# Kernel tuning notes

Measured on AMD Instinct MI355X. Metric: run time of the kernel, lower is better.

The kernel has to match this reference:

```python
import jax, jax.numpy as jnp
import numpy as np

N = 500_000      # num nodes
E = 8_000_000    # num edges (before self-loops)
F_IN, H, C = 16, 8, 2


def setup_inputs() -> dict:
    key = jax.random.key(0)
    k = jax.random.split(key, 6)
    x = jax.random.normal(k[0], (N, F_IN), dtype=jnp.float32)
    edge_index = jax.random.randint(k[1], (2, E), 0, N, dtype=jnp.int32)
    # Glorot-style init like PyG GCNConv
    W1 = jax.random.normal(k[2], (F_IN, H), dtype=jnp.float32) * (1.0 / np.sqrt(F_IN))
    b1 = jnp.zeros((H,), dtype=jnp.float32)
    W2 = jax.random.normal(k[3], (H, C), dtype=jnp.float32) * (1.0 / np.sqrt(H))
    b2 = jnp.zeros((C,), dtype=jnp.float32)
    return {"x": x, "W1": W1, "b1": b1, "W2": W2, "b2": b2, "edge_index": edge_index}


def reference(x, W1, b1, W2, b2, edge_index):
    # GCNConv: out = D^{-1/2} (A + I) D^{-1/2} X W + b   (PyG semantics)
    row, col = edge_index[0], edge_index[1]           # messages flow row -> col
    loop = jnp.arange(N, dtype=row.dtype)
    row = jnp.concatenate([row, loop])                # add self-loops
    col = jnp.concatenate([col, loop])
    deg = jax.ops.segment_sum(jnp.ones_like(col, dtype=x.dtype), col, num_segments=N)
    dinv = jnp.where(deg > 0, jax.lax.rsqrt(deg), jnp.zeros_like(deg))
    norm = dinv[row] * dinv[col]                      # [E+N]

    def propagate(h):  # h: [N, d] -> normalized scatter-add aggregation
        msg = h[row] * norm[:, None]                  # gather + scale, [E+N, d]
        return jax.ops.segment_sum(msg, col, num_segments=N)

    h = jax.nn.relu(propagate(x @ W1) + b1)           # [N, 8]
    out = propagate(h @ W2) + b2                      # [N, 2]
    return jax.nn.log_softmax(out, axis=1)
```

## Files before the change

### kernel.cpp

```cpp
#include <hip/hip_runtime.h>

#define TPB 256
#define NBLK_EDGE 1024
#define CHUNKE 8192
#define BIN_SHIFT 9
#define BIN_SIZE 512
#define MAXK 1024
#define ROW_BITS 19
#define ROW_MASK ((1u << ROW_BITS) - 1)
#define Q_SHIFT 17
#define NKEY 2048
#define CAP 12288

typedef _Float16 half8  __attribute__((ext_vector_type(8)));
typedef _Float16 half2v __attribute__((ext_vector_type(2)));

__global__ void k_hist(const int* __restrict__ col, int E, int chunk, int K,
                       int* __restrict__ cntB, int* __restrict__ cntT) {
    __shared__ int lh[MAXK];
    int blk = blockIdx.x;
    for (int k = threadIdx.x; k < MAXK; k += blockDim.x) lh[k] = 0;
    __syncthreads();
    int s = blk * chunk, e_ = min(s + chunk, E);
    for (int e = s + threadIdx.x; e < e_; e += blockDim.x)
        atomicAdd(&lh[col[e] >> BIN_SHIFT], 1);
    __syncthreads();
    for (int k = threadIdx.x; k < MAXK; k += blockDim.x) {
        int v = lh[k];
        cntB[(size_t)blk * MAXK + k] = v;
        cntT[(size_t)k * NBLK_EDGE + blk] = v;
    }
}

__global__ void k_colscan(int* __restrict__ cntT, int* __restrict__ ghist) {
    __shared__ int part[256];
    int b = blockIdx.x, tid = threadIdx.x;
    size_t base = (size_t)b * NBLK_EDGE;
    int t4 = tid * 4;
    int c0 = cntT[base + t4], c1 = cntT[base + t4 + 1],
        c2 = cntT[base + t4 + 2], c3 = cntT[base + t4 + 3];
    int sum = c0 + c1 + c2 + c3;
    part[tid] = sum;
    __syncthreads();
    for (int off = 1; off < 256; off <<= 1) {
        int v = (tid >= off) ? part[tid - off] : 0;
        __syncthreads();
        part[tid] += v;
        __syncthreads();
    }
    int excl = part[tid] - sum;
    cntT[base + t4]     = excl;
    cntT[base + t4 + 1] = excl + c0;
    cntT[base + t4 + 2] = excl + c0 + c1;
    cntT[base + t4 + 3] = excl + c0 + c1 + c2;
    if (tid == 255) ghist[b] = part[255];
}

__global__ void k_scan(const int* __restrict__ ghist, int K, int* __restrict__ binBase,
                       int* __restrict__ scratchCur) {
    __shared__ int tmp[MAXK];
    int tid = threadIdx.x;
    if (tid == 0) *scratchCur = 0;
    int val = (tid < K) ? ghist[tid] : 0;
    tmp[tid] = val;
    __syncthreads();
    for (int off = 1; off < MAXK; off <<= 1) {
        int v = (tid >= off) ? tmp[tid - off] : 0;
        __syncthreads();
        tmp[tid] += v;
        __syncthreads();
    }
    int incl = tmp[tid];
    if (tid < K) binBase[tid] = incl - val;
    if (tid == K - 1) binBase[K] = incl;
}

__global__ void __launch_bounds__(1024) k_reorder(
        const int* __restrict__ row, const int* __restrict__ col,
        int E, int chunk, int K,
        const int* __restrict__ binBase, const int* __restrict__ cntB,
        const int* __restrict__ cntT, unsigned* __restrict__ packed) {
    __shared__ unsigned sorted[CHUNKE];
    __shared__ unsigned short sbin[CHUNKE];
    __shared__ int lcur[MAXK], lbase[MAXK], gbase[MAXK];
    __shared__ int part[1024];
    int blk = blockIdx.x, tid = threadIdx.x;
    int s = blk * chunk, e_ = min(s + chunk, E), len = e_ - s;
    size_t bb = (size_t)blk * MAXK;
    int c0 = cntB[bb + tid];
    part[tid] = c0;
    __syncthreads();
    for (int off = 1; off < 1024; off <<= 1) {
        int v = (tid >= off) ? part[tid - off] : 0;
        __syncthreads();
        part[tid] += v;
        __syncthreads();
    }
    int excl = part[tid] - c0;
    lbase[tid] = excl;
    lcur[tid] = excl;
    gbase[tid] = binBase[tid] + cntT[(size_t)tid * NBLK_EDGE + blk];
    __syncthreads();
    for (int i = tid; i < len; i += blockDim.x) {
        int cc = col[s + i];
        int b = cc >> BIN_SHIFT;
        int slot = atomicAdd(&lcur[b], 1);
        sorted[slot] = ((unsigned)(cc & (BIN_SIZE - 1)) << ROW_BITS) | (unsigned)row[s + i];
        sbin[slot] = (unsigned short)b;
    }
    __syncthreads();
    for (int i = tid; i < len; i += blockDim.x) {
        int b = sbin[i];
        packed[gbase[b] + (i - lbase[b])] = sorted[i];
    }
}

__global__ void __launch_bounds__(1024) k_binsort_deg(
        unsigned* __restrict__ packed, const int* __restrict__ binBase,
        unsigned* __restrict__ scratch, int* __restrict__ scratchCur,
        const float* __restrict__ x, const float* __restrict__ W1,
        float* __restrict__ dinv, half8* __restrict__ g0,
        int* __restrict__ keyptr, int N, int E, int K) {
    __shared__ unsigned buf2[CAP];
    __shared__ int cnt[NKEY], cur[NKEY];
    __shared__ int part[1024];
    __shared__ int sbShared;
    int tid = threadIdx.x;
    int bin = blockIdx.x;
    int s = binBase[bin], t = binBase[bin + 1];
    int len = t - s;
    bool fast = (len <= CAP);
    cnt[tid] = 0;
    cnt[tid + 1024] = 0;
    if (!fast && tid == 0) sbShared = atomicAdd(scratchCur, len);
    __syncthreads();
    for (int i = tid; i < len; i += blockDim.x) {
        unsigned v = packed[s + i];
        int k = (int)((v >> ROW_BITS) << 2) | (int)((v & ROW_MASK) >> Q_SHIFT);
        atomicAdd(&cnt[k], 1);
    }
    __syncthreads();
    int t2 = tid * 2;
    int c0 = cnt[t2], c1 = cnt[t2 + 1];
    int sum = c0 + c1;
    part[tid] = sum;
    __syncthreads();
    for (int off = 1; off < 1024; off <<= 1) {
        int v = (tid >= off) ? part[tid - off] : 0;
        __syncthreads();
        part[tid] += v;
        __syncthreads();
    }
    int excl = part[tid] - sum;
    cur[t2] = excl;
    cur[t2 + 1] = excl + c0;
    int base = bin << BIN_SHIFT;
    if (base + (t2 >> 2) < N) keyptr[((size_t)bin << 11) + t2] = s + excl;
    if (base + ((t2 + 1) >> 2) < N) keyptr[((size_t)bin << 11) + t2 + 1] = s + excl + c0;
    float di = 0.0f;
    int node = base + tid;
    if (tid < BIN_SIZE && node < N) {
        int deg = cnt[4 * tid] + cnt[4 * tid + 1] + cnt[4 * tid + 2] + cnt[4 * tid + 3];
        di = rsqrtf((float)(deg + 1));
        dinv[node] = di;
    }
    if (bin == K - 1 && tid == 0) keyptr[(size_t)4 * N] = E;
    __syncthreads();
    if (fast) {
        for (int i = tid; i < len; i += blockDim.x) {
            unsigned v = packed[s + i];
            int k = (int)((v >> ROW_BITS) << 2) | (int)((v & ROW_MASK) >> Q_SHIFT);
            int slot = atomicAdd(&cur[k], 1);
            buf2[slot] = v;
        }
        __syncthreads();
        for (int i = tid; i < len; i += blockDim.x) packed[s + i] = buf2[i];
    } else {
        unsigned* stg = scratch + sbShared;
        for (int i = tid; i < len; i += blockDim.x) stg[i] = packed[s + i];
        __threadfence();
        __syncthreads();
        for (int i = tid; i < len; i += blockDim.x) {
            unsigned v = stg[i];
            int k = (int)((v >> ROW_BITS) << 2) | (int)((v & ROW_MASK) >> Q_SHIFT);
            int slot = atomicAdd(&cur[k], 1);
            packed[s + slot] = v;
        }
    }
    if (tid < BIN_SIZE && node < N) {
        const float4* xv = (const float4*)(x + (size_t)node * 16);
        float h[8];
#pragma unroll
        for (int j = 0; j < 8; ++j) h[j] = 0.0f;
#pragma unroll
        for (int kk = 0; kk < 4; ++kk) {
            float4 a = xv[kk];
            int kb = kk * 4;
#pragma unroll
            for (int j = 0; j < 8; ++j)
                h[j] += a.x * W1[kb * 8 + j] + a.y * W1[(kb + 1) * 8 + j]
                      + a.z * W1[(kb + 2) * 8 + j] + a.w * W1[(kb + 3) * 8 + j];
        }
        half8 g;
#pragma unroll
        for (int j = 0; j < 8; ++j) g[j] = (_Float16)(di * h[j]);
        g0[node] = g;
    }
}

__global__ void k_gather1_phase(const unsigned* __restrict__ packed,
                                const int* __restrict__ keyptr,
                                const half8* __restrict__ g0,
                                const float* __restrict__ dinv_arr,
                                const float* __restrict__ b1,
                                const float* __restrict__ W2,
                                float* __restrict__ accA,
                                half2v* __restrict__ g1, int N, int q) {
    int i = blockIdx.x * blockDim.x + threadIdx.x;
    if (i >= N) return;
    int s = keyptr[4 * i + q], t = keyptr[4 * i + q + 1];
    float acc[8];
    if (q == 0) {
#pragma unroll
        for (int j = 0; j < 8; ++j) acc[j] = 0.0f;
    } else {
        const float4* av = (const float4*)(accA + (size_t)i * 8);
        float4 lo = av[0], hi = av[1];
        acc[0] = lo.x; acc[1] = lo.y; acc[2] = lo.z; acc[3] = lo.w;
        acc[4] = hi.x; acc[5] = hi.y; acc[6] = hi.z; acc[7] = hi.w;
    }
    int e = s;
    for (; e + 4 <= t; e += 4) {
        unsigned p0 = packed[e], p1 = packed[e + 1], p2 = packed[e + 2], p3 = packed[e + 3];
        half8 v0 = g0[p0 & ROW_MASK];
        half8 v1 = g0[p1 & ROW_MASK];
        half8 v2 = g0[p2 & ROW_MASK];
        half8 v3 = g0[p3 & ROW_MASK];
#pragma unroll
        for (int j = 0; j < 8; ++j)
            acc[j] += (float)v0[j] + (float)v1[j] + (float)v2[j] + (float)v3[j];
    }
    for (; e < t; ++e) {
        half8 v = g0[packed[e] & ROW_MASK];
#pragma unroll
        for (int j = 0; j < 8; ++j) acc[j] += (float)v[j];
    }
    if (q < 3) {
        float4* av = (float4*)(accA + (size_t)i * 8);
        av[0] = make_float4(acc[0], acc[1], acc[2], acc[3]);
        av[1] = make_float4(acc[4], acc[5], acc[6], acc[7]);
    } else {
        half8 self = g0[i];
        float di = dinv_arr[i];
        float o0 = 0.0f, o1 = 0.0f;
#pragma unroll
        for (int j = 0; j < 8; ++j) {
            float hj = fmaxf(di * (acc[j] + (float)self[j]) + b1[j], 0.0f);
            o0 += hj * W2[j * 2 + 0];
            o1 += hj * W2[j * 2 + 1];
        }
        half2v g;
        g.x = (_Float16)(di * o0);
        g.y = (_Float16)(di * o1);
        g1[i] = g;
    }
}

__global__ void k_gather2_final(const unsigned* __restrict__ packed,
                                const int* __restrict__ keyptr,
                                const half2v* __restrict__ g1,
                                const float* __restrict__ dinv_arr,
                                const float* __restrict__ b2,
                                float* __restrict__ out, int N) {
    int i = blockIdx.x * blockDim.x + threadIdx.x;
    if (i >= N) return;
    int s = keyptr[4 * i], t = keyptr[4 * i + 4];
    half2v sg = g1[i];
    float a0 = (float)sg.x, a1 = (float)sg.y;
    int e = s;
    for (; e + 4 <= t; e += 4) {
        unsigned p0 = packed[e], p1 = packed[e + 1], p2 = packed[e + 2], p3 = packed[e + 3];
        half2v v0 = g1[p0 & ROW_MASK];
        half2v v1 = g1[p1 & ROW_MASK];
        half2v v2 = g1[p2 & ROW_MASK];
        half2v v3 = g1[p3 & ROW_MASK];
        a0 += (float)v0.x + (float)v1.x + (float)v2.x + (float)v3.x;
        a1 += (float)v0.y + (float)v1.y + (float)v2.y + (float)v3.y;
    }
    for (; e < t; ++e) {
        half2v v = g1[packed[e] & ROW_MASK];
        a0 += (float)v.x;
        a1 += (float)v.y;
    }
    float di = dinv_arr[i];
    float o0 = di * a0 + b2[0];
    float o1 = di * a1 + b2[1];
    float m = fmaxf(o0, o1);
    float lse = m + logf(expf(o0 - m) + expf(o1 - m));
    ((float2*)out)[i] = make_float2(o0 - lse, o1 - lse);
}

extern "C" void kernel_launch(void* const* d_in, const int* in_sizes, int n_in,
                              void* d_out, int out_size, void* d_ws, size_t ws_size,
                              hipStream_t stream) {
    const float* x  = (const float*)d_in[0];
    const float* W1 = (const float*)d_in[1];
    const float* b1 = (const float*)d_in[2];
    const float* W2 = (const float*)d_in[3];
    const float* b2 = (const float*)d_in[4];
    const int*   ei = (const int*)d_in[5];

    const int N = in_sizes[0] / 16;
    const int E = in_sizes[5] / 2;
    const int* row = ei;
    const int* col = ei + E;
    const int K = (N + BIN_SIZE - 1) >> BIN_SHIFT;

    float* ws   = (float*)d_ws;
    float* dinv = ws;
    half8* g0   = (half8*)(ws + (size_t)N);
    half2v* g1  = (half2v*)(ws + (size_t)5 * N);
    float* accA = ws + (size_t)6 * N;
    int* keyptr = (int*)(ws + (size_t)14 * N);
    int*   meta = (int*)(ws + (size_t)18 * N + 8);
    int* ghist      = meta;
    int* binBase    = meta + MAXK;
    int* scratchCur = meta + 2 * MAXK + 16;
    unsigned* packed = (unsigned*)(meta + 3 * MAXK);
    int* cntB = (int*)(packed + E);
    int* cntT = cntB + (size_t)MAXK * NBLK_EDGE;

    float* out = (float*)d_out;

    const int gN = (N + TPB - 1) / TPB;
    const int chunk = (E + NBLK_EDGE - 1) / NBLK_EDGE;

    k_hist       <<<NBLK_EDGE, TPB, 0, stream>>>(col, E, chunk, K, cntB, cntT);
    k_colscan    <<<K, 256, 0, stream>>>(cntT, ghist);
    k_scan       <<<1, MAXK, 0, stream>>>(ghist, K, binBase, scratchCur);
    k_reorder    <<<NBLK_EDGE, 1024, 0, stream>>>(row, col, E, chunk, K,
                                                  binBase, cntB, cntT, packed);
    k_binsort_deg<<<K, 1024, 0, stream>>>(packed, binBase, (unsigned*)accA, scratchCur,
                                          x, W1, dinv, g0, keyptr, N, E, K);
    for (int q = 0; q < 4; ++q)
        k_gather1_phase<<<gN, TPB, 0, stream>>>(packed, keyptr, g0, dinv, b1, W2,
                                                accA, g1, N, q);
    k_gather2_final<<<gN, TPB, 0, stream>>>(packed, keyptr, g1, dinv, b2, out, N);
}
```

Measured before the change: 371.9 us.

## Fuse gather phases into one cooperative kernel and use wave-shuffle block scans

Replaces the four per-quarter gather launches and the final gather with one cooperative kernel. It keeps accumulators in registers across grid.sync barriers, recomputes dinv from keyptr, and runs the second propagation plus log_softmax in the same kernel. This removes the accA global read/write round trips and several launches. The Hillis-Steele shared-memory scans become wave-shuffle scans, and the edge-chunk block count is halved with bigger chunks and 1024-thread histogram blocks. The cost is grid-wide barriers, and the kernel relies on every block being co-resident; if occupancy is too low it falls back to the old path.

Result: faster. 356.7 us (-4.1%).

```diff
diff --git a/kernel.cpp b/kernel.cpp
--- a/kernel.cpp
+++ b/kernel.cpp
@@ -1,8 +1,11 @@
 #include <hip/hip_runtime.h>
+#include <hip/hip_cooperative_groups.h>
+
+namespace cg = cooperative_groups;
 
 #define TPB 256
-#define NBLK_EDGE 1024
-#define CHUNKE 8192
+#define NBLK_EDGE 512
+#define CHUNKE 16384
 #define BIN_SHIFT 9
 #define BIN_SIZE 512
 #define MAXK 1024
@@ -15,6 +18,33 @@
 typedef _Float16 half8  __attribute__((ext_vector_type(8)));
 typedef _Float16 half2v __attribute__((ext_vector_type(2)));
 
+__device__ __forceinline__ int wave_scan_incl(int v, int lane) {
+#pragma unroll
+    for (int d = 1; d < 64; d <<= 1) {
+        int u = __shfl_up(v, d, 64);
+        if (lane >= d) v += u;
+    }
+    return v;
+}
+
+__device__ __forceinline__ int block_excl_scan_1024(int v, int tid, int* wsum) {
+    int lane = tid & 63, wv = tid >> 6;
+    int incl = wave_scan_incl(v, lane);
+    if (lane == 63) wsum[wv] = incl;
+    __syncthreads();
+    if (tid < 16) {
+        int w = wsum[tid];
+#pragma unroll
+        for (int d = 1; d < 16; d <<= 1) {
+            int u = __shfl_up(w, d, 16);
+            if (tid >= d) w += u;
+        }
+        wsum[tid] = w;
+    }
+    __syncthreads();
+    return incl - v + (wv ? wsum[wv - 1] : 0);
+}
+
 __global__ void k_hist(const int* __restrict__ col, int E, int chunk, int K,
                        int* __restrict__ cntB, int* __restrict__ cntT) {
     __shared__ int lh[MAXK];
@@ -36,10 +66,9 @@
     __shared__ int part[256];
     int b = blockIdx.x, tid = threadIdx.x;
     size_t base = (size_t)b * NBLK_EDGE;
-    int t4 = tid * 4;
-    int c0 = cntT[base + t4], c1 = cntT[base + t4 + 1],
-        c2 = cntT[base + t4 + 2], c3 = cntT[base + t4 + 3];
-    int sum = c0 + c1 + c2 + c3;
+    int t2 = tid * 2;
+    int c0 = cntT[base + t2], c1 = cntT[base + t2 + 1];
+    int sum = c0 + c1;
     part[tid] = sum;
     __syncthreads();
     for (int off = 1; off < 256; off <<= 1) {
@@ -49,30 +78,20 @@
         __syncthreads();
     }
     int excl = part[tid] - sum;
-    cntT[base + t4]     = excl;
-    cntT[base + t4 + 1] = excl + c0;
-    cntT[base + t4 + 2] = excl + c0 + c1;
-    cntT[base + t4 + 3] = excl + c0 + c1 + c2;
+    cntT[base + t2]     = excl;
+    cntT[base + t2 + 1] = excl + c0;
     if (tid == 255) ghist[b] = part[255];
 }
 
 __global__ void k_scan(const int* __restrict__ ghist, int K, int* __restrict__ binBase,
                        int* __restrict__ scratchCur) {
-    __shared__ int tmp[MAXK];
+    __shared__ int wsum[16];
     int tid = threadIdx.x;
     if (tid == 0) *scratchCur = 0;
     int val = (tid < K) ? ghist[tid] : 0;
-    tmp[tid] = val;
-    __syncthreads();
-    for (int off = 1; off < MAXK; off <<= 1) {
-        int v = (tid >= off) ? tmp[tid - off] : 0;
-        __syncthreads();
-        tmp[tid] += v;
-        __syncthreads();
-    }
-    int incl = tmp[tid];
-    if (tid < K) binBase[tid] = incl - val;
-    if (tid == K - 1) binBase[K] = incl;
+    int excl = block_excl_scan_1024(val, tid, wsum);
+    if (tid < K) binBase[tid] = excl;
+    if (tid == K - 1) binBase[K] = excl + val;
 }
 
 __global__ void __launch_bounds__(1024) k_reorder(
@@ -83,20 +102,12 @@
     __shared__ unsigned sorted[CHUNKE];
     __shared__ unsigned short sbin[CHUNKE];
     __shared__ int lcur[MAXK], lbase[MAXK], gbase[MAXK];
-    __shared__ int part[1024];
+    __shared__ int wsum[16];
     int blk = blockIdx.x, tid = threadIdx.x;
     int s = blk * chunk, e_ = min(s + chunk, E), len = e_ - s;
     size_t bb = (size_t)blk * MAXK;
     int c0 = cntB[bb + tid];
-    part[tid] = c0;
-    __syncthreads();
-    for (int off = 1; off < 1024; off <<= 1) {
-        int v = (tid >= off) ? part[tid - off] : 0;
-        __syncthreads();
-        part[tid] += v;
-        __syncthreads();
-    }
-    int excl = part[tid] - c0;
+    int excl = block_excl_scan_1024(c0, tid, wsum);
     lbase[tid] = excl;
     lcur[tid] = excl;
     gbase[tid] = binBase[tid] + cntT[(size_t)tid * NBLK_EDGE + blk];
@@ -123,7 +134,7 @@
         int* __restrict__ keyptr, int N, int E, int K) {
     __shared__ unsigned buf2[CAP];
     __shared__ int cnt[NKEY], cur[NKEY];
-    __shared__ int part[1024];
+    __shared__ int wsum[16];
     __shared__ int sbShared;
     int tid = threadIdx.x;
     int bin = blockIdx.x;
@@ -143,15 +154,7 @@
     int t2 = tid * 2;
     int c0 = cnt[t2], c1 = cnt[t2 + 1];
     int sum = c0 + c1;
-    part[tid] = sum;
-    __syncthreads();
-    for (int off = 1; off < 1024; off <<= 1) {
-        int v = (tid >= off) ? part[tid - off] : 0;
-        __syncthreads();
-        part[tid] += v;
-        __syncthreads();
-    }
-    int excl = part[tid] - sum;
+    int excl = block_excl_scan_1024(sum, tid, wsum);
     cur[t2] = excl;
     cur[t2 + 1] = excl + c0;
     int base = bin << BIN_SHIFT;
@@ -205,6 +208,95 @@
 #pragma unroll
         for (int j = 0; j < 8; ++j) g[j] = (_Float16)(di * h[j]);
         g0[node] = g;
+    }
+}
+
+__device__ __forceinline__ void gather_g0_range(const unsigned* __restrict__ packed,
+                                                const half8* __restrict__ g0,
+                                                int e, int t, float* acc) {
+    for (; e + 4 <= t; e += 4) {
+        unsigned p0 = packed[e], p1 = packed[e + 1], p2 = packed[e + 2], p3 = packed[e + 3];
+        half8 v0 = g0[p0 & ROW_MASK];
+        half8 v1 = g0[p1 & ROW_MASK];
+        half8 v2 = g0[p2 & ROW_MASK];
+        half8 v3 = g0[p3 & ROW_MASK];
+#pragma unroll
+        for (int j = 0; j < 8; ++j)
+            acc[j] += (float)v0[j] + (float)v1[j] + (float)v2[j] + (float)v3[j];
+    }
+    for (; e < t; ++e) {
+        half8 v = g0[packed[e] & ROW_MASK];
+#pragma unroll
+        for (int j = 0; j < 8; ++j) acc[j] += (float)v[j];
+    }
+}
+
+__global__ void __launch_bounds__(TPB, 8) k_gather_fused(
+        const unsigned* __restrict__ packed, const int* __restrict__ keyptr,
+        const half8* __restrict__ g0, const float* __restrict__ b1,
+        const float* __restrict__ W2, const float* __restrict__ b2,
+        half2v* __restrict__ g1, float* __restrict__ out, int N) {
+    cg::grid_group grid = cg::this_grid();
+    int i = blockIdx.x * blockDim.x + threadIdx.x;
+    bool act = (i < N);
+    int kp0 = 0, kp1 = 0, kp2 = 0, kp3 = 0, kp4 = 0;
+    float acc[8];
+#pragma unroll
+    for (int j = 0; j < 8; ++j) acc[j] = 0.0f;
+    if (act) {
+        int4 k4 = ((const int4*)keyptr)[i];
+        kp0 = k4.x; kp1 = k4.y; kp2 = k4.z; kp3 = k4.w;
+        kp4 = keyptr[4 * i + 4];
+    }
+    if (act) gather_g0_range(packed, g0, kp0, kp1, acc);
+    grid.sync();
+    if (act) gather_g0_range(packed, g0, kp1, kp2, acc);
+    grid.sync();
+    if (act) gather_g0_range(packed, g0, kp2, kp3, acc);
+    grid.sync();
+    if (act) gather_g0_range(packed, g0, kp3, kp4, acc);
+    float di = 0.0f, s0 = 0.0f, s1 = 0.0f;
+    if (act) {
+        half8 self = g0[i];
+        di = rsqrtf((float)(kp4 - kp0 + 1));
+        float o0 = 0.0f, o1 = 0.0f;
+#pragma unroll
+        for (int j = 0; j < 8; ++j) {
+            float hj = fmaxf(di * (acc[j] + (float)self[j]) + b1[j], 0.0f);
+            o0 += hj * W2[j * 2 + 0];
+            o1 += hj * W2[j * 2 + 1];
+        }
+        s0 = di * o0;
+        s1 = di * o1;
+        half2v g;
+        g.x = (_Float16)s0;
+        g.y = (_Float16)s1;
+        g1[i] = g;
+    }
+    __threadfence();
+    grid.sync();
+    if (act) {
+        float a0 = s0, a1 = s1;
+        int e = kp0, t = kp4;
+        for (; e + 4 <= t; e += 4) {
+            unsigned p0 = packed[e], p1 = packed[e + 1], p2 = packed[e + 2], p3 = packed[e + 3];
+            half2v v0 = g1[p0 & ROW_MASK];
+            half2v v1 = g1[p1 & ROW_MASK];
+            half2v v2 = g1[p2 & ROW_MASK];
+            half2v v3 = g1[p3 & ROW_MASK];
+            a0 += (float)v0.x + (float)v1.x + (float)v2.x + (float)v3.x;
+            a1 += (float)v0.y + (float)v1.y + (float)v2.y + (float)v3.y;
+        }
+        for (; e < t; ++e) {
+            half2v v = g1[packed[e] & ROW_MASK];
+            a0 += (float)v.x;
+            a1 += (float)v.y;
+        }
+        float o0 = di * a0 + b2[0];
+        float o1 = di * a1 + b2[1];
+        float m = fmaxf(o0, o1);
+        float lse = m + logf(expf(o0 - m) + expf(o1 - m));
+        ((float2*)out)[i] = make_float2(o0 - lse, o1 - lse);
     }
 }
 
@@ -229,22 +321,7 @@
         acc[0] = lo.x; acc[1] = lo.y; acc[2] = lo.z; acc[3] = lo.w;
         acc[4] = hi.x; acc[5] = hi.y; acc[6] = hi.z; acc[7] = hi.w;
     }
-    int e = s;
-    for (; e + 4 <= t; e += 4) {
-        unsigned p0 = packed[e], p1 = packed[e + 1], p2 = packed[e + 2], p3 = packed[e + 3];
-        half8 v0 = g0[p0 & ROW_MASK];
-        half8 v1 = g0[p1 & ROW_MASK];
-        half8 v2 = g0[p2 & ROW_MASK];
-        half8 v3 = g0[p3 & ROW_MASK];
-#pragma unroll
-        for (int j = 0; j < 8; ++j)
-            acc[j] += (float)v0[j] + (float)v1[j] + (float)v2[j] + (float)v3[j];
-    }
-    for (; e < t; ++e) {
-        half8 v = g0[packed[e] & ROW_MASK];
-#pragma unroll
-        for (int j = 0; j < 8; ++j) acc[j] += (float)v[j];
-    }
+    gather_g0_range(packed, g0, s, t, acc);
     if (q < 3) {
         float4* av = (float4*)(accA + (size_t)i * 8);
         av[0] = make_float4(acc[0], acc[1], acc[2], acc[3]);
@@ -335,15 +412,34 @@
     const int gN = (N + TPB - 1) / TPB;
     const int chunk = (E + NBLK_EDGE - 1) / NBLK_EDGE;
 
-    k_hist       <<<NBLK_EDGE, TPB, 0, stream>>>(col, E, chunk, K, cntB, cntT);
+    static int coop_capacity = -1;
+    if (coop_capacity < 0) {
+        int nb = 0;
+        if (hipOccupancyMaxActiveBlocksPerMultiprocessor(&nb, k_gather_fused, TPB, 0)
+            != hipSuccess) nb = 0;
+        hipDeviceProp_t prop;
+        int ncu = 0;
+        if (hipGetDeviceProperties(&prop, 0) == hipSuccess) ncu = prop.multiProcessorCount;
+        coop_capacity = nb * ncu;
+    }
+
+    k_hist       <<<NBLK_EDGE, 1024, 0, stream>>>(col, E, chunk, K, cntB, cntT);
     k_colscan    <<<K, 256, 0, stream>>>(cntT, ghist);
     k_scan       <<<1, MAXK, 0, stream>>>(ghist, K, binBase, scratchCur);
     k_reorder    <<<NBLK_EDGE, 1024, 0, stream>>>(row, col, E, chunk, K,
                                                   binBase, cntB, cntT, packed);
     k_binsort_deg<<<K, 1024, 0, stream>>>(packed, binBase, (unsigned*)accA, scratchCur,
                                           x, W1, dinv, g0, keyptr, N, E, K);
-    for (int q = 0; q < 4; ++q)
-        k_gather1_phase<<<gN, TPB, 0, stream>>>(packed, keyptr, g0, dinv, b1, W2,
-                                                accA, g1, N, q);
-    k_gather2_final<<<gN, TPB, 0, stream>>>(packed, keyptr, g1, dinv, b2, out, N);
-}
+    if (coop_capacity >= gN) {
+        int nN = N;
+        void* cargs[] = {(void*)&packed, (void*)&keyptr, (void*)&g0, (void*)&b1,
+                         (void*)&W2, (void*)&b2, (void*)&g1, (void*)&out, (void*)&nN};
+        hipLaunchCooperativeKernel(k_gather_fused, dim3(gN), dim3(TPB),
+                                   cargs, 0, stream);
+    } else {
+        for (int q = 0; q < 4; ++q)
+            k_gather1_phase<<<gN, TPB, 0, stream>>>(packed, keyptr, g0, dinv, b1, W2,
+                                                    accA, g1, N, q);
+        k_gather2_final<<<gN, TPB, 0, stream>>>(packed, keyptr, g1, dinv, b2, out, N);
+    }
+}
```

## Replace per-node CSR sort with per-bin shared-memory atomic aggregation

Applied to the files above, without the earlier changes.

Drops the second-level within-bin sort and the keyptr CSR. Edges are now only coarsely binned by destination into 1024-node bins, and each bin's block accumulates messages with LDS float atomics for both propagation layers. This removes the binsort pass, the four phased gather launches and the accA round trips. It also swaps the shared-memory Hillis-Steele scans for wave-shuffle scans and retunes chunk and bin sizes. In exchange there are many more LDS atomics (8 per edge in layer 1), and the float summation order is no longer deterministic.

Result: slower. 613.1 us (+64.8%).

```diff
diff --git a/kernel.cpp b/kernel.cpp
--- a/kernel.cpp
+++ b/kernel.cpp
@@ -1,22 +1,46 @@
 #include <hip/hip_runtime.h>
 
-#define TPB 256
-#define NBLK_EDGE 1024
-#define CHUNKE 8192
-#define BIN_SHIFT 9
-#define BIN_SIZE 512
+#define NBLK_EDGE 768
+#define CHUNKE 10432
+#define BIN_SHIFT 10
+#define BIN_SIZE 1024
 #define MAXK 1024
 #define ROW_BITS 19
 #define ROW_MASK ((1u << ROW_BITS) - 1)
-#define Q_SHIFT 17
-#define NKEY 2048
-#define CAP 12288
 
 typedef _Float16 half8  __attribute__((ext_vector_type(8)));
 typedef _Float16 half2v __attribute__((ext_vector_type(2)));
 
-__global__ void k_hist(const int* __restrict__ col, int E, int chunk, int K,
-                       int* __restrict__ cntB, int* __restrict__ cntT) {
+__device__ __forceinline__ int wave_scan_incl(int v, int lane) {
+#pragma unroll
+    for (int d = 1; d < 64; d <<= 1) {
+        int u = __shfl_up(v, d, 64);
+        if (lane >= d) v += u;
+    }
+    return v;
+}
+
+__device__ __forceinline__ int block_excl_scan_1024(int v, int tid, int* wsum) {
+    int lane = tid & 63, wv = tid >> 6;
+    int incl = wave_scan_incl(v, lane);
+    if (lane == 63) wsum[wv] = incl;
+    __syncthreads();
+    if (tid < 16) {
+        int w = wsum[tid];
+#pragma unroll
+        for (int d = 1; d < 16; d <<= 1) {
+            int u = __shfl_up(w, d, 16);
+            if (tid >= d) w += u;
+        }
+        wsum[tid] = w;
+    }
+    __syncthreads();
+    return incl - v + (wv ? wsum[wv - 1] : 0);
+}
+
+__global__ void __launch_bounds__(1024) k_hist(
+        const int* __restrict__ col, int E, int chunk, int K,
+        int* __restrict__ cntB, int* __restrict__ cntT) {
     __shared__ int lh[MAXK];
     int blk = blockIdx.x;
     for (int k = threadIdx.x; k < MAXK; k += blockDim.x) lh[k] = 0;
@@ -36,10 +60,9 @@
     __shared__ int part[256];
     int b = blockIdx.x, tid = threadIdx.x;
     size_t base = (size_t)b * NBLK_EDGE;
-    int t4 = tid * 4;
-    int c0 = cntT[base + t4], c1 = cntT[base + t4 + 1],
-        c2 = cntT[base + t4 + 2], c3 = cntT[base + t4 + 3];
-    int sum = c0 + c1 + c2 + c3;
+    int t3 = tid * 3;
+    int c0 = cntT[base + t3], c1 = cntT[base + t3 + 1], c2 = cntT[base + t3 + 2];
+    int sum = c0 + c1 + c2;
     part[tid] = sum;
     __syncthreads();
     for (int off = 1; off < 256; off <<= 1) {
@@ -49,30 +72,19 @@
         __syncthreads();
     }
     int excl = part[tid] - sum;
-    cntT[base + t4]     = excl;
-    cntT[base + t4 + 1] = excl + c0;
-    cntT[base + t4 + 2] = excl + c0 + c1;
-    cntT[base + t4 + 3] = excl + c0 + c1 + c2;
+    cntT[base + t3]     = excl;
+    cntT[base + t3 + 1] = excl + c0;
+    cntT[base + t3 + 2] = excl + c0 + c1;
     if (tid == 255) ghist[b] = part[255];
 }
 
-__global__ void k_scan(const int* __restrict__ ghist, int K, int* __restrict__ binBase,
-                       int* __restrict__ scratchCur) {
-    __shared__ int tmp[MAXK];
+__global__ void k_scan(const int* __restrict__ ghist, int K, int* __restrict__ binBase) {
+    __shared__ int wsum[16];
     int tid = threadIdx.x;
-    if (tid == 0) *scratchCur = 0;
     int val = (tid < K) ? ghist[tid] : 0;
-    tmp[tid] = val;
-    __syncthreads();
-    for (int off = 1; off < MAXK; off <<= 1) {
-        int v = (tid >= off) ? tmp[tid - off] : 0;
-        __syncthreads();
-        tmp[tid] += v;
-        __syncthreads();
-    }
-    int incl = tmp[tid];
-    if (tid < K) binBase[tid] = incl - val;
-    if (tid == K - 1) binBase[K] = incl;
+    int excl = block_excl_scan_1024(val, tid, wsum);
+    if (tid < K) binBase[tid] = excl;
+    if (tid == K - 1) binBase[K] = excl + val;
 }
 
 __global__ void __launch_bounds__(1024) k_reorder(
@@ -83,20 +95,12 @@
     __shared__ unsigned sorted[CHUNKE];
     __shared__ unsigned short sbin[CHUNKE];
     __shared__ int lcur[MAXK], lbase[MAXK], gbase[MAXK];
-    __shared__ int part[1024];
+    __shared__ int wsum[16];
     int blk = blockIdx.x, tid = threadIdx.x;
     int s = blk * chunk, e_ = min(s + chunk, E), len = e_ - s;
     size_t bb = (size_t)blk * MAXK;
     int c0 = cntB[bb + tid];
-    part[tid] = c0;
-    __syncthreads();
-    for (int off = 1; off < 1024; off <<= 1) {
-        int v = (tid >= off) ? part[tid - off] : 0;
-        __syncthreads();
-        part[tid] += v;
-        __syncthreads();
-    }
-    int excl = part[tid] - c0;
+    int excl = block_excl_scan_1024(c0, tid, wsum);
     lbase[tid] = excl;
     lcur[tid] = excl;
     gbase[tid] = binBase[tid] + cntT[(size_t)tid * NBLK_EDGE + blk];
@@ -115,79 +119,24 @@
     }
 }
 
-__global__ void __launch_bounds__(1024) k_binsort_deg(
-        unsigned* __restrict__ packed, const int* __restrict__ binBase,
-        unsigned* __restrict__ scratch, int* __restrict__ scratchCur,
+__global__ void __launch_bounds__(1024) k_degmlp(
+        const unsigned* __restrict__ packed, const int* __restrict__ binBase,
         const float* __restrict__ x, const float* __restrict__ W1,
-        float* __restrict__ dinv, half8* __restrict__ g0,
-        int* __restrict__ keyptr, int N, int E, int K) {
-    __shared__ unsigned buf2[CAP];
-    __shared__ int cnt[NKEY], cur[NKEY];
-    __shared__ int part[1024];
-    __shared__ int sbShared;
-    int tid = threadIdx.x;
-    int bin = blockIdx.x;
+        float* __restrict__ dinv, half8* __restrict__ g0, int N) {
+    __shared__ int cnt[BIN_SIZE];
+    __shared__ float w1s[128];
+    int tid = threadIdx.x, bin = blockIdx.x;
+    cnt[tid] = 0;
+    if (tid < 128) w1s[tid] = W1[tid];
+    __syncthreads();
     int s = binBase[bin], t = binBase[bin + 1];
-    int len = t - s;
-    bool fast = (len <= CAP);
-    cnt[tid] = 0;
-    cnt[tid + 1024] = 0;
-    if (!fast && tid == 0) sbShared = atomicAdd(scratchCur, len);
-    __syncthreads();
-    for (int i = tid; i < len; i += blockDim.x) {
-        unsigned v = packed[s + i];
-        int k = (int)((v >> ROW_BITS) << 2) | (int)((v & ROW_MASK) >> Q_SHIFT);
-        atomicAdd(&cnt[k], 1);
-    }
-    __syncthreads();
-    int t2 = tid * 2;
-    int c0 = cnt[t2], c1 = cnt[t2 + 1];
-    int sum = c0 + c1;
-    part[tid] = sum;
-    __syncthreads();
-    for (int off = 1; off < 1024; off <<= 1) {
-        int v = (tid >= off) ? part[tid - off] : 0;
-        __syncthreads();
-        part[tid] += v;
-        __syncthreads();
-    }
-    int excl = part[tid] - sum;
-    cur[t2] = excl;
-    cur[t2 + 1] = excl + c0;
-    int base = bin << BIN_SHIFT;
-    if (base + (t2 >> 2) < N) keyptr[((size_t)bin << 11) + t2] = s + excl;
-    if (base + ((t2 + 1) >> 2) < N) keyptr[((size_t)bin << 11) + t2 + 1] = s + excl + c0;
-    float di = 0.0f;
-    int node = base + tid;
-    if (tid < BIN_SIZE && node < N) {
-        int deg = cnt[4 * tid] + cnt[4 * tid + 1] + cnt[4 * tid + 2] + cnt[4 * tid + 3];
-        di = rsqrtf((float)(deg + 1));
+    for (int i = s + tid; i < t; i += 1024)
+        atomicAdd(&cnt[packed[i] >> ROW_BITS], 1);
+    __syncthreads();
+    int node = (bin << BIN_SHIFT) + tid;
+    if (node < N) {
+        float di = rsqrtf((float)(cnt[tid] + 1));
         dinv[node] = di;
-    }
-    if (bin == K - 1 && tid == 0) keyptr[(size_t)4 * N] = E;
-    __syncthreads();
-    if (fast) {
-        for (int i = tid; i < len; i += blockDim.x) {
-            unsigned v = packed[s + i];
-            int k = (int)((v >> ROW_BITS) << 2) | (int)((v & ROW_MASK) >> Q_SHIFT);
-            int slot = atomicAdd(&cur[k], 1);
-            buf2[slot] = v;
-        }
-        __syncthreads();
-        for (int i = tid; i < len; i += blockDim.x) packed[s + i] = buf2[i];
-    } else {
-        unsigned* stg = scratch + sbShared;
-        for (int i = tid; i < len; i += blockDim.x) stg[i] = packed[s + i];
-        __threadfence();
-        __syncthreads();
-        for (int i = tid; i < len; i += blockDim.x) {
-            unsigned v = stg[i];
-            int k = (int)((v >> ROW_BITS) << 2) | (int)((v & ROW_MASK) >> Q_SHIFT);
-            int slot = atomicAdd(&cur[k], 1);
-            packed[s + slot] = v;
-        }
-    }
-    if (tid < BIN_SIZE && node < N) {
         const float4* xv = (const float4*)(x + (size_t)node * 16);
         float h[8];
 #pragma unroll
@@ -198,8 +147,8 @@
             int kb = kk * 4;
 #pragma unroll
             for (int j = 0; j < 8; ++j)
-                h[j] += a.x * W1[kb * 8 + j] + a.y * W1[(kb + 1) * 8 + j]
-                      + a.z * W1[(kb + 2) * 8 + j] + a.w * W1[(kb + 3) * 8 + j];
+                h[j] += a.x * w1s[kb * 8 + j] + a.y * w1s[(kb + 1) * 8 + j]
+                      + a.z * w1s[(kb + 2) * 8 + j] + a.w * w1s[(kb + 3) * 8 + j];
         }
         half8 g;
 #pragma unroll
@@ -208,96 +157,71 @@
     }
 }
 
-__global__ void k_gather1_phase(const unsigned* __restrict__ packed,
-                                const int* __restrict__ keyptr,
-                                const half8* __restrict__ g0,
-                                const float* __restrict__ dinv_arr,
-                                const float* __restrict__ b1,
-                                const float* __restrict__ W2,
-                                float* __restrict__ accA,
-                                half2v* __restrict__ g1, int N, int q) {
-    int i = blockIdx.x * blockDim.x + threadIdx.x;
-    if (i >= N) return;
-    int s = keyptr[4 * i + q], t = keyptr[4 * i + q + 1];
-    float acc[8];
-    if (q == 0) {
-#pragma unroll
-        for (int j = 0; j < 8; ++j) acc[j] = 0.0f;
-    } else {
-        const float4* av = (const float4*)(accA + (size_t)i * 8);
-        float4 lo = av[0], hi = av[1];
-        acc[0] = lo.x; acc[1] = lo.y; acc[2] = lo.z; acc[3] = lo.w;
-        acc[4] = hi.x; acc[5] = hi.y; acc[6] = hi.z; acc[7] = hi.w;
-    }
-    int e = s;
-    for (; e + 4 <= t; e += 4) {
-        unsigned p0 = packed[e], p1 = packed[e + 1], p2 = packed[e + 2], p3 = packed[e + 3];
-        half8 v0 = g0[p0 & ROW_MASK];
-        half8 v1 = g0[p1 & ROW_MASK];
-        half8 v2 = g0[p2 & ROW_MASK];
-        half8 v3 = g0[p3 & ROW_MASK];
-#pragma unroll
-        for (int j = 0; j < 8; ++j)
-            acc[j] += (float)v0[j] + (float)v1[j] + (float)v2[j] + (float)v3[j];
-    }
-    for (; e < t; ++e) {
-        half8 v = g0[packed[e] & ROW_MASK];
-#pragma unroll
-        for (int j = 0; j < 8; ++j) acc[j] += (float)v[j];
-    }
-    if (q < 3) {
-        float4* av = (float4*)(accA + (size_t)i * 8);
-        av[0] = make_float4(acc[0], acc[1], acc[2], acc[3]);
-        av[1] = make_float4(acc[4], acc[5], acc[6], acc[7]);
-    } else {
-        half8 self = g0[i];
-        float di = dinv_arr[i];
+__global__ void __launch_bounds__(1024) k_g1(
+        const unsigned* __restrict__ packed, const int* __restrict__ binBase,
+        const half8* __restrict__ g0, const float* __restrict__ dinv,
+        const float* __restrict__ b1, const float* __restrict__ W2,
+        half2v* __restrict__ g1, int N) {
+    __shared__ float acc[8][BIN_SIZE];
+    int tid = threadIdx.x, bin = blockIdx.x;
+#pragma unroll
+    for (int j = 0; j < 8; ++j) acc[j][tid] = 0.0f;
+    __syncthreads();
+    int s = binBase[bin], t = binBase[bin + 1];
+    for (int i = s + tid; i < t; i += 1024) {
+        unsigned v = packed[i];
+        int d = (int)(v >> ROW_BITS);
+        half8 sv = g0[v & ROW_MASK];
+#pragma unroll
+        for (int j = 0; j < 8; ++j) atomicAdd(&acc[j][d], (float)sv[j]);
+    }
+    __syncthreads();
+    int node = (bin << BIN_SHIFT) + tid;
+    if (node < N) {
+        float di = dinv[node];
+        half8 self = g0[node];
         float o0 = 0.0f, o1 = 0.0f;
 #pragma unroll
         for (int j = 0; j < 8; ++j) {
-            float hj = fmaxf(di * (acc[j] + (float)self[j]) + b1[j], 0.0f);
+            float hj = fmaxf(di * (acc[j][tid] + (float)self[j]) + b1[j], 0.0f);
             o0 += hj * W2[j * 2 + 0];
             o1 += hj * W2[j * 2 + 1];
         }
         half2v g;
         g.x = (_Float16)(di * o0);
         g.y = (_Float16)(di * o1);
-        g1[i] = g;
-    }
-}
-
-__global__ void k_gather2_final(const unsigned* __restrict__ packed,
-                                const int* __restrict__ keyptr,
-                                const half2v* __restrict__ g1,
-                                const float* __restrict__ dinv_arr,
-                                const float* __restrict__ b2,
-                                float* __restrict__ out, int N) {
-    int i = blockIdx.x * blockDim.x + threadIdx.x;
-    if (i >= N) return;
-    int s = keyptr[4 * i], t = keyptr[4 * i + 4];
-    half2v sg = g1[i];
-    float a0 = (float)sg.x, a1 = (float)sg.y;
-    int e = s;
-    for (; e + 4 <= t; e += 4) {
-        unsigned p0 = packed[e], p1 = packed[e + 1], p2 = packed[e + 2], p3 = packed[e + 3];
-        half2v v0 = g1[p0 & ROW_MASK];
-        half2v v1 = g1[p1 & ROW_MASK];
-        half2v v2 = g1[p2 & ROW_MASK];
-        half2v v3 = g1[p3 & ROW_MASK];
-        a0 += (float)v0.x + (float)v1.x + (float)v2.x + (float)v3.x;
-        a1 += (float)v0.y + (float)v1.y + (float)v2.y + (float)v3.y;
-    }
-    for (; e < t; ++e) {
-        half2v v = g1[packed[e] & ROW_MASK];
-        a0 += (float)v.x;
-        a1 += (float)v.y;
-    }
-    float di = dinv_arr[i];
-    float o0 = di * a0 + b2[0];
-    float o1 = di * a1 + b2[1];
-    float m = fmaxf(o0, o1);
-    float lse = m + logf(expf(o0 - m) + expf(o1 - m));
-    ((float2*)out)[i] = make_float2(o0 - lse, o1 - lse);
+        g1[node] = g;
+    }
+}
+
+__global__ void __launch_bounds__(1024) k_g2(
+        const unsigned* __restrict__ packed, const int* __restrict__ binBase,
+        const half2v* __restrict__ g1, const float* __restrict__ dinv,
+        const float* __restrict__ b2, float* __restrict__ out, int N) {
+    __shared__ float acc0[BIN_SIZE], acc1[BIN_SIZE];
+    int tid = threadIdx.x, bin = blockIdx.x;
+    acc0[tid] = 0.0f;
+    acc1[tid] = 0.0f;
+    __syncthreads();
+    int s = binBase[bin], t = binBase[bin + 1];
+    for (int i = s + tid; i < t; i += 1024) {
+        unsigned v = packed[i];
+        int d = (int)(v >> ROW_BITS);
+        half2v sv = g1[v & ROW_MASK];
+        atomicAdd(&acc0[d], (float)sv.x);
+        atomicAdd(&acc1[d], (float)sv.y);
+    }
+    __syncthreads();
+    int node = (bin << BIN_SHIFT) + tid;
+    if (node < N) {
+        float di = dinv[node];
+        half2v self = g1[node];
+        float o0 = di * (acc0[tid] + (float)self.x) + b2[0];
+        float o1 = di * (acc1[tid] + (float)self.y) + b2[1];
+        float m = fmaxf(o0, o1);
+        float lse = m + logf(expf(o0 - m) + expf(o1 - m));
+        ((float2*)out)[node] = make_float2(o0 - lse, o1 - lse);
+    }
 }
 
 extern "C" void kernel_launch(void* const* d_in, const int* in_sizes, int n_in,
@@ -320,30 +244,23 @@
     float* dinv = ws;
     half8* g0   = (half8*)(ws + (size_t)N);
     half2v* g1  = (half2v*)(ws + (size_t)5 * N);
-    float* accA = ws + (size_t)6 * N;
-    int* keyptr = (int*)(ws + (size_t)14 * N);
-    int*   meta = (int*)(ws + (size_t)18 * N + 8);
+    int*   meta = (int*)(ws + (size_t)6 * N);
     int* ghist      = meta;
     int* binBase    = meta + MAXK;
-    int* scratchCur = meta + 2 * MAXK + 16;
     unsigned* packed = (unsigned*)(meta + 3 * MAXK);
     int* cntB = (int*)(packed + E);
     int* cntT = cntB + (size_t)MAXK * NBLK_EDGE;
 
     float* out = (float*)d_out;
 
-    const int gN = (N + TPB - 1) / TPB;
     const int chunk = (E + NBLK_EDGE - 1) / NBLK_EDGE;
 
-    k_hist       <<<NBLK_EDGE, TPB, 0, stream>>>(col, E, chunk, K, cntB, cntT);
-    k_colscan    <<<K, 256, 0, stream>>>(cntT, ghist);
-    k_scan       <<<1, MAXK, 0, stream>>>(ghist, K, binBase, scratchCur);
-    k_reorder    <<<NBLK_EDGE, 1024, 0, stream>>>(row, col, E, chunk, K,
-                                                  binBase, cntB, cntT, packed);
-    k_binsort_deg<<<K, 1024, 0, stream>>>(packed, binBase, (unsigned*)accA, scratchCur,
-                                          x, W1, dinv, g0, keyptr, N, E, K);
-    for (int q = 0; q < 4; ++q)
-        k_gather1_phase<<<gN, TPB, 0, stream>>>(packed, keyptr, g0, dinv, b1, W2,
-                                                accA, g1, N, q);
-    k_gather2_final<<<gN, TPB, 0, stream>>>(packed, keyptr, g1, dinv, b2, out, N);
-}
+    k_hist   <<<NBLK_EDGE, 1024, 0, stream>>>(col, E, chunk, K, cntB, cntT);
+    k_colscan<<<K, 256, 0, stream>>>(cntT, ghist);
+    k_scan   <<<1, MAXK, 0, stream>>>(ghist, K, binBase);
+    k_reorder<<<NBLK_EDGE, 1024, 0, stream>>>(row, col, E, chunk, K,
+                                              binBase, cntB, cntT, packed);
+    k_degmlp <<<K, 1024, 0, stream>>>(packed, binBase, x, W1, dinv, g0, N);
+    k_g1     <<<K, 1024, 0, stream>>>(packed, binBase, g0, dinv, b1, W2, g1, N);
+    k_g2     <<<K, 1024, 0, stream>>>(packed, binBase, g1, dinv, b2, out, N);
+}
```
